# Kernel optimization log

Measured on AMD Instinct MI355X. Metric: run time of the kernel, lower is better.

## Reference

```python
import jax, jax.numpy as jnp
import numpy as np
from jax import lax

NUM_STEPS = 20
BATCH, DIM, HID = 4096, 512, 2048


def setup_inputs() -> dict:
    key = jax.random.key(0)
    k_z, k_w1, k_w2 = jax.random.split(key, 3)
    z0 = jax.random.normal(k_z, (BATCH, DIM), dtype=jnp.float32)
    # fan-in scaled weights so the ODE dynamics stay well-conditioned
    W1 = jax.random.normal(k_w1, (DIM + 1, HID), dtype=jnp.float32) * (1.0 / np.sqrt(DIM + 1))
    b1 = jnp.zeros((HID,), dtype=jnp.float32)
    W2 = jax.random.normal(k_w2, (HID, DIM), dtype=jnp.float32) * (0.1 / np.sqrt(HID))
    b2 = jnp.zeros((DIM,), dtype=jnp.float32)
    t0 = jnp.zeros((), dtype=jnp.float32)
    t1 = jnp.ones((), dtype=jnp.float32)
    return {"z0": z0, "W1": W1, "b1": b1, "W2": W2, "b2": b2, "t0": t0, "t1": t1}


def reference(z0, W1, b1, W2, b2, t0, t1):
    h = (t1 - t0) / NUM_STEPS

    def func(z, t):
        # time broadcast to [batch, 1], concatenated to the state (Neural-ODE MLP dynamics)
        tb = jnp.full((z.shape[0], 1), t, dtype=z.dtype)
        hidden = jnp.tanh(jnp.concatenate([z, tb], axis=-1) @ W1 + b1)
        return hidden @ W2 + b2

    def step(z, i):
        t = t0 + i * h
        k1 = func(z, t)
        k2 = func(z + 0.5 * h * k1, t + 0.5 * h)
        k3 = func(z + 0.5 * h * k2, t + 0.5 * h)
        k4 = func(z + h * k3, t + h)
        z_next = z + (h / 6.0) * (k1 + 2.0 * k2 + 2.0 * k3 + k4)
        return z_next, None

    z, _ = lax.scan(step, z0, jnp.arange(NUM_STEPS, dtype=z0.dtype))
    return z
```

## Files before the change

kernel.cpp:

```cpp
#include <hip/hip_runtime.h>
#include <hip/hip_bf16.h>

#define BATCH 4096
#define DIM   512
#define HID   2048
#define NSTEPS 20

typedef __attribute__((ext_vector_type(8))) short short8;
typedef __attribute__((ext_vector_type(4))) short short4v;
typedef __attribute__((ext_vector_type(4))) float floatx4;

#define GLL(dst, src) __builtin_amdgcn_global_load_lds( \
    (const __attribute__((address_space(1))) void*)(src), \
    (__attribute__((address_space(3))) void*)(dst), 16, 0, 0)

__device__ __forceinline__ short f2bf(float x) {
    union { float f; unsigned u; } v; v.f = x;
    unsigned r = v.u + 0x7fffu + ((v.u >> 16) & 1u);
    return (short)(r >> 16);
}

__device__ __forceinline__ float fast_tanh(float x) {
    float e = __builtin_amdgcn_exp2f(x * 2.8853900817779268f);
    float r = __builtin_amdgcn_rcpf(1.0f + e);
    return 1.0f - 2.0f * r;
}

__global__ void transpose_cvt(const float* __restrict__ src, short* __restrict__ dst,
                              int K, int N) {
    __shared__ float tile[32][33];
    int k0 = blockIdx.x * 32, n0 = blockIdx.y * 32;
    int tx = threadIdx.x, ty = threadIdx.y;
    #pragma unroll
    for (int r = ty; r < 32; r += 8)
        tile[r][tx] = src[(size_t)(k0 + r) * N + n0 + tx];
    __syncthreads();
    #pragma unroll
    for (int r = ty; r < 32; r += 8)
        dst[(size_t)(n0 + r) * K + k0 + tx] = f2bf(tile[tx][r]);
}

__global__ void extract_row(const float* __restrict__ W1, float* __restrict__ w1last) {
    int i = blockIdx.x * 256 + threadIdx.x;
    w1last[i] = W1[(size_t)DIM * HID + i];
}

__global__ void init_abuf(const float* __restrict__ z0, short* __restrict__ abuf) {
    size_t i = (size_t)(blockIdx.x * 256 + threadIdx.x) * 4;
    float4 zv = *(const float4*)(z0 + i);
    short4v o;
    o[0] = f2bf(zv.x); o[1] = f2bf(zv.y); o[2] = f2bf(zv.z); o[3] = f2bf(zv.w);
    *(short4v*)(abuf + i) = o;
}

__global__ __launch_bounds__(256, 4)
void gemm1_tanh(const short* __restrict__ A, const short* __restrict__ Bt,
                const float* __restrict__ b1, const float* __restrict__ w1last,
                const float* __restrict__ t0p, const float* __restrict__ t1p,
                float c_t, float step_i,
                short* __restrict__ hidden) {
    __shared__ short Alds[128 * 64];
    __shared__ short Blds[64 * 64];
    const int tid = threadIdx.x;
    const int lane = tid & 63;
    const int wave = tid >> 6;
    const int wm = wave >> 1, wn = wave & 1;
    const int bm0 = blockIdx.x * 128;
    const int bn0 = blockIdx.y * 64;

    const float t0 = t0p[0], t1 = t1p[0];
    const float h = (t1 - t0) / (float)NSTEPS;
    const float teval = t0 + (step_i + c_t) * h;

    floatx4 acc[4][2];
    #pragma unroll
    for (int i = 0; i < 4; i++) {
        acc[i][0] = (floatx4)0.f;
        acc[i][1] = (floatx4)0.f;
    }

    const int fr = lane & 15;
    const int fkc = lane >> 4;
    const int rx = fr & 7;

    for (int kk = 0; kk < DIM; kk += 64) {
        #pragma unroll
        for (int p = 0; p < 4; p++) {
            int c = tid + p * 256;
            int row = c >> 3;
            int g = (c & 7) ^ (row & 7);
            GLL(&Alds[c * 8], A + (size_t)(bm0 + row) * DIM + kk + g * 8);
        }
        #pragma unroll
        for (int p = 0; p < 2; p++) {
            int c = tid + p * 256;
            int row = c >> 3;
            int g = (c & 7) ^ (row & 7);
            GLL(&Blds[c * 8], Bt + (size_t)(bn0 + row) * DIM + kk + g * 8);
        }
        __syncthreads();
        #pragma unroll
        for (int s = 0; s < 2; s++) {
            const int slot = ((s * 4 + fkc) ^ rx) * 8;
            short8 bfr[2];
            #pragma unroll
            for (int nt = 0; nt < 2; nt++)
                bfr[nt] = *(const short8*)&Blds[(wn * 32 + nt * 16 + fr) * 64 + slot];
            #pragma unroll
            for (int mt = 0; mt < 4; mt++) {
                short8 af = *(const short8*)&Alds[(wm * 64 + mt * 16 + fr) * 64 + slot];
                #pragma unroll
                for (int nt = 0; nt < 2; nt++)
                    acc[mt][nt] = __builtin_amdgcn_mfma_f32_16x16x32_bf16(bfr[nt], af, acc[mt][nt], 0, 0, 0);
            }
        }
        __syncthreads();
    }
    #pragma unroll
    for (int mt = 0; mt < 4; mt++) {
        int m = bm0 + wm * 64 + mt * 16 + fr;
        short* hrow = hidden + (size_t)m * HID;
        #pragma unroll
        for (int nt = 0; nt < 2; nt++) {
            int n0 = bn0 + wn * 32 + nt * 16 + fkc * 4;
            float4 bb = *(const float4*)&b1[n0];
            float4 wl = *(const float4*)&w1last[n0];
            short4v o;
            o[0] = f2bf(fast_tanh(acc[mt][nt][0] + bb.x + teval * wl.x));
            o[1] = f2bf(fast_tanh(acc[mt][nt][1] + bb.y + teval * wl.y));
            o[2] = f2bf(fast_tanh(acc[mt][nt][2] + bb.z + teval * wl.z));
            o[3] = f2bf(fast_tanh(acc[mt][nt][3] + bb.w + teval * wl.w));
            *(short4v*)&hrow[n0] = o;
        }
    }
}

__global__ __launch_bounds__(256, 2)
void gemm2_fused(const short* __restrict__ hidden,
                 const short* __restrict__ Bt,
                 const float* __restrict__ b2,
                 float* __restrict__ z,
                 float* __restrict__ kacc, short* __restrict__ abuf,
                 const float* __restrict__ t0p, const float* __restrict__ t1p,
                 int mode, float wk, float alpha_c) {
    __shared__ short lds[4 * 8192];
    const int tid = threadIdx.x;
    const int lane = tid & 63;
    const int wave = tid >> 6;
    const int bm0 = blockIdx.x * 64;
    const int bn0 = blockIdx.y * 64;
    const int kbase = wave * 512;

    short* slabA = &lds[wave * 8192];
    short* slabB = slabA + 4096;

    const int fr = lane & 15;
    const int fkc = lane >> 4;
    const int rx = fr & 7;
    const int l3 = lane >> 3;
    const int gch = (lane & 7) ^ l3;

    floatx4 acc[4][4];
    #pragma unroll
    for (int i = 0; i < 4; i++)
        #pragma unroll
        for (int j = 0; j < 4; j++) acc[i][j] = (floatx4)0.f;

    for (int kk = 0; kk < 512; kk += 64) {
        const int k0 = kbase + kk;
        __builtin_amdgcn_s_waitcnt(0xC07F);
        #pragma unroll
        for (int j = 0; j < 8; j++) {
            int row = j * 8 + l3;
            GLL(&slabA[j * 512 + lane * 8], hidden + (size_t)(bm0 + row) * HID + k0 + gch * 8);
            GLL(&slabB[j * 512 + lane * 8], Bt     + (size_t)(bn0 + row) * HID + k0 + gch * 8);
        }
        __builtin_amdgcn_sched_barrier(0);
        __builtin_amdgcn_s_waitcnt(0x0F70);
        __builtin_amdgcn_sched_barrier(0);
        #pragma unroll
        for (int s = 0; s < 2; s++) {
            const int slot = ((s * 4 + fkc) ^ rx) * 8;
            short8 af[4], bfr[4];
            #pragma unroll
            for (int mt = 0; mt < 4; mt++)
                af[mt] = *(const short8*)&slabA[(mt * 16 + fr) * 64 + slot];
            #pragma unroll
            for (int nt = 0; nt < 4; nt++)
                bfr[nt] = *(const short8*)&slabB[(nt * 16 + fr) * 64 + slot];
            #pragma unroll
            for (int mt = 0; mt < 4; mt++)
                #pragma unroll
                for (int nt = 0; nt < 4; nt++)
                    acc[mt][nt] = __builtin_amdgcn_mfma_f32_16x16x32_bf16(af[mt], bfr[nt], acc[mt][nt], 0, 0, 0);
        }
        __builtin_amdgcn_sched_barrier(0);
    }

    float* fslab = (float*)slabA;
    #pragma unroll
    for (int mt = 0; mt < 4; mt++)
        #pragma unroll
        for (int nt = 0; nt < 4; nt++)
            #pragma unroll
            for (int r = 0; r < 4; r++) {
                int row = mt * 16 + fkc * 4 + r;
                int col = nt * 16 + fr;
                fslab[row * 64 + col] = acc[mt][nt][r];
            }
    __syncthreads();

    const int rrow = tid >> 2;
    const int cb = (tid & 3) * 16;
    float4 v[4];
    #pragma unroll
    for (int ch = 0; ch < 4; ch++) v[ch] = make_float4(0.f, 0.f, 0.f, 0.f);
    #pragma unroll
    for (int w = 0; w < 4; w++) {
        const float* fs = (const float*)&lds[w * 8192];
        #pragma unroll
        for (int ch = 0; ch < 4; ch++) {
            float4 p = *(const float4*)&fs[rrow * 64 + cb + ch * 4];
            v[ch].x += p.x; v[ch].y += p.y; v[ch].z += p.z; v[ch].w += p.w;
        }
    }

    const float h = (t1p[0] - t0p[0]) / (float)NSTEPS;
    const float ah = alpha_c * h;
    const float h6 = h / 6.0f;
    const size_t base = (size_t)(bm0 + rrow) * DIM + bn0 + cb;
    #pragma unroll
    for (int ch = 0; ch < 4; ch++) {
        float4 bb = *(const float4*)&b2[bn0 + cb + ch * 4];
        float kv[4] = { v[ch].x + bb.x, v[ch].y + bb.y, v[ch].z + bb.z, v[ch].w + bb.w };
        size_t idx = base + ch * 4;
        float4 zv = *(const float4*)&z[idx];
        float zn[4];
        if (mode == 0) {
            *(float4*)&kacc[idx] = make_float4(kv[0], kv[1], kv[2], kv[3]);
            zn[0] = zv.x + ah * kv[0]; zn[1] = zv.y + ah * kv[1];
            zn[2] = zv.z + ah * kv[2]; zn[3] = zv.w + ah * kv[3];
        } else if (mode == 1) {
            float4 ka = *(const float4*)&kacc[idx];
            *(float4*)&kacc[idx] = make_float4(ka.x + wk * kv[0], ka.y + wk * kv[1],
                                               ka.z + wk * kv[2], ka.w + wk * kv[3]);
            zn[0] = zv.x + ah * kv[0]; zn[1] = zv.y + ah * kv[1];
            zn[2] = zv.z + ah * kv[2]; zn[3] = zv.w + ah * kv[3];
        } else {
            float4 ka = *(const float4*)&kacc[idx];
            zn[0] = zv.x + h6 * (ka.x + kv[0]); zn[1] = zv.y + h6 * (ka.y + kv[1]);
            zn[2] = zv.z + h6 * (ka.z + kv[2]); zn[3] = zv.w + h6 * (ka.w + kv[3]);
            *(float4*)&z[idx] = make_float4(zn[0], zn[1], zn[2], zn[3]);
        }
        short4v o;
        o[0] = f2bf(zn[0]); o[1] = f2bf(zn[1]); o[2] = f2bf(zn[2]); o[3] = f2bf(zn[3]);
        *(short4v*)&abuf[idx] = o;
    }
}

extern "C" void kernel_launch(void* const* d_in, const int* in_sizes, int n_in,
                              void* d_out, int out_size, void* d_ws, size_t ws_size,
                              hipStream_t stream) {
    const float* z0  = (const float*)d_in[0];
    const float* W1  = (const float*)d_in[1];
    const float* b1  = (const float*)d_in[2];
    const float* W2  = (const float*)d_in[3];
    const float* b2  = (const float*)d_in[4];
    const float* t0p = (const float*)d_in[5];
    const float* t1p = (const float*)d_in[6];
    float* z = (float*)d_out;

    char* ws = (char*)d_ws;
    short* W1t    = (short*)(ws);
    short* W2t    = (short*)(ws + (2u << 20));
    float* w1last = (float*)(ws + (4u << 20));
    short* abuf   = (short*)(ws + (4u << 20) + (1u << 16));
    short* hidden = (short*)(ws + (8u << 20) + (1u << 16));
    float* kacc   = (float*)(ws + (24u << 20) + (1u << 16));

    hipMemcpyAsync(z, z0, (size_t)BATCH * DIM * sizeof(float),
                   hipMemcpyDeviceToDevice, stream);
    transpose_cvt<<<dim3(DIM / 32, HID / 32), dim3(32, 8), 0, stream>>>(W1, W1t, DIM, HID);
    transpose_cvt<<<dim3(HID / 32, DIM / 32), dim3(32, 8), 0, stream>>>(W2, W2t, HID, DIM);
    extract_row<<<HID / 256, 256, 0, stream>>>(W1, w1last);
    init_abuf<<<BATCH * DIM / 4 / 256, 256, 0, stream>>>(z0, abuf);

    const dim3 g1(BATCH / 128, HID / 64), g2(BATCH / 64, DIM / 64), b(256);
    for (int i = 0; i < NSTEPS; i++) {
        float fi = (float)i;
        gemm1_tanh<<<g1, b, 0, stream>>>(abuf, W1t, b1, w1last, t0p, t1p, 0.0f, fi, hidden);
        gemm2_fused<<<g2, b, 0, stream>>>(hidden, W2t, b2, z, kacc, abuf, t0p, t1p, 0, 1.0f, 0.5f);
        gemm1_tanh<<<g1, b, 0, stream>>>(abuf, W1t, b1, w1last, t0p, t1p, 0.5f, fi, hidden);
        gemm2_fused<<<g2, b, 0, stream>>>(hidden, W2t, b2, z, kacc, abuf, t0p, t1p, 1, 2.0f, 0.5f);
        gemm1_tanh<<<g1, b, 0, stream>>>(abuf, W1t, b1, w1last, t0p, t1p, 0.5f, fi, hidden);
        gemm2_fused<<<g2, b, 0, stream>>>(hidden, W2t, b2, z, kacc, abuf, t0p, t1p, 1, 2.0f, 1.0f);
        gemm1_tanh<<<g1, b, 0, stream>>>(abuf, W1t, b1, w1last, t0p, t1p, 1.0f, fi, hidden);
        gemm2_fused<<<g2, b, 0, stream>>>(hidden, W2t, b2, z, kacc, abuf, t0p, t1p, 2, 1.0f, 0.0f);
    }
}
```

Baseline: 3.145 ms.

## Enlarge gemm1 tiles to 128x128x128 and split gemm2 K across eight waves

gemm1_tanh now computes a 128x128 output tile per block with a 128-wide K step, so each wave holds a 4x4 MFMA accumulator grid. This raises arithmetic intensity and halves the number of blocks, at the cost of more LDS (64KB) and registers, which lowers occupancy. gemm2_fused now uses 512 threads with eight waves each covering 256 of K instead of four covering 512, with an eight-way LDS reduction. That shortens the serial per-wave K loop, adds reduction work, and doubles the LDS footprint.

```diff
diff --git a/kernel.cpp b/kernel.cpp
--- a/kernel.cpp
+++ b/kernel.cpp
@@ -53,66 +53,62 @@
     *(short4v*)(abuf + i) = o;
 }
 
-__global__ __launch_bounds__(256, 4)
+__global__ __launch_bounds__(256, 2)
 void gemm1_tanh(const short* __restrict__ A, const short* __restrict__ Bt,
                 const float* __restrict__ b1, const float* __restrict__ w1last,
                 const float* __restrict__ t0p, const float* __restrict__ t1p,
                 float c_t, float step_i,
                 short* __restrict__ hidden) {
-    __shared__ short Alds[128 * 64];
-    __shared__ short Blds[64 * 64];
+    __shared__ short Alds[128 * 128];
+    __shared__ short Blds[128 * 128];
     const int tid = threadIdx.x;
     const int lane = tid & 63;
     const int wave = tid >> 6;
     const int wm = wave >> 1, wn = wave & 1;
     const int bm0 = blockIdx.x * 128;
-    const int bn0 = blockIdx.y * 64;
+    const int bn0 = blockIdx.y * 128;
 
     const float t0 = t0p[0], t1 = t1p[0];
     const float h = (t1 - t0) / (float)NSTEPS;
     const float teval = t0 + (step_i + c_t) * h;
 
-    floatx4 acc[4][2];
-    #pragma unroll
-    for (int i = 0; i < 4; i++) {
-        acc[i][0] = (floatx4)0.f;
-        acc[i][1] = (floatx4)0.f;
-    }
+    floatx4 acc[4][4];
+    #pragma unroll
+    for (int i = 0; i < 4; i++)
+        #pragma unroll
+        for (int j = 0; j < 4; j++) acc[i][j] = (floatx4)0.f;
 
     const int fr = lane & 15;
     const int fkc = lane >> 4;
     const int rx = fr & 7;
 
-    for (int kk = 0; kk < DIM; kk += 64) {
-        #pragma unroll
-        for (int p = 0; p < 4; p++) {
+    for (int kk = 0; kk < DIM; kk += 128) {
+        #pragma unroll
+        for (int p = 0; p < 8; p++) {
             int c = tid + p * 256;
-            int row = c >> 3;
-            int g = (c & 7) ^ (row & 7);
-            GLL(&Alds[c * 8], A + (size_t)(bm0 + row) * DIM + kk + g * 8);
-        }
-        #pragma unroll
-        for (int p = 0; p < 2; p++) {
-            int c = tid + p * 256;
-            int row = c >> 3;
-            int g = (c & 7) ^ (row & 7);
+            int row = c >> 4;
+            int ci = c & 15;
+            int g = ((ci & 7) ^ (row & 7)) | (ci & 8);
+            GLL(&Alds[c * 8], A  + (size_t)(bm0 + row) * DIM + kk + g * 8);
             GLL(&Blds[c * 8], Bt + (size_t)(bn0 + row) * DIM + kk + g * 8);
         }
         __syncthreads();
         #pragma unroll
-        for (int s = 0; s < 2; s++) {
-            const int slot = ((s * 4 + fkc) ^ rx) * 8;
-            short8 bfr[2];
-            #pragma unroll
-            for (int nt = 0; nt < 2; nt++)
-                bfr[nt] = *(const short8*)&Blds[(wn * 32 + nt * 16 + fr) * 64 + slot];
-            #pragma unroll
-            for (int mt = 0; mt < 4; mt++) {
-                short8 af = *(const short8*)&Alds[(wm * 64 + mt * 16 + fr) * 64 + slot];
+        for (int s = 0; s < 4; s++) {
+            const int lc = s * 4 + fkc;
+            const int slot = ((((lc & 7) ^ rx) | (lc & 8))) * 8;
+            short8 af[4], bfr[4];
+            #pragma unroll
+            for (int mt = 0; mt < 4; mt++)
+                af[mt] = *(const short8*)&Alds[(wm * 64 + mt * 16 + fr) * 128 + slot];
+            #pragma unroll
+            for (int nt = 0; nt < 4; nt++)
+                bfr[nt] = *(const short8*)&Blds[(wn * 64 + nt * 16 + fr) * 128 + slot];
+            #pragma unroll
+            for (int mt = 0; mt < 4; mt++)
                 #pragma unroll
-                for (int nt = 0; nt < 2; nt++)
-                    acc[mt][nt] = __builtin_amdgcn_mfma_f32_16x16x32_bf16(bfr[nt], af, acc[mt][nt], 0, 0, 0);
-            }
+                for (int nt = 0; nt < 4; nt++)
+                    acc[mt][nt] = __builtin_amdgcn_mfma_f32_16x16x32_bf16(bfr[nt], af[mt], acc[mt][nt], 0, 0, 0);
         }
         __syncthreads();
     }
@@ -121,8 +117,8 @@
         int m = bm0 + wm * 64 + mt * 16 + fr;
         short* hrow = hidden + (size_t)m * HID;
         #pragma unroll
-        for (int nt = 0; nt < 2; nt++) {
-            int n0 = bn0 + wn * 32 + nt * 16 + fkc * 4;
+        for (int nt = 0; nt < 4; nt++) {
+            int n0 = bn0 + wn * 64 + nt * 16 + fkc * 4;
             float4 bb = *(const float4*)&b1[n0];
             float4 wl = *(const float4*)&w1last[n0];
             short4v o;
@@ -135,7 +131,7 @@
     }
 }
 
-__global__ __launch_bounds__(256, 2)
+__global__ __launch_bounds__(512, 2)
 void gemm2_fused(const short* __restrict__ hidden,
                  const short* __restrict__ Bt,
                  const float* __restrict__ b2,
@@ -143,13 +139,13 @@
                  float* __restrict__ kacc, short* __restrict__ abuf,
                  const float* __restrict__ t0p, const float* __restrict__ t1p,
                  int mode, float wk, float alpha_c) {
-    __shared__ short lds[4 * 8192];
+    __shared__ short lds[8 * 8192];
     const int tid = threadIdx.x;
     const int lane = tid & 63;
     const int wave = tid >> 6;
     const int bm0 = blockIdx.x * 64;
     const int bn0 = blockIdx.y * 64;
-    const int kbase = wave * 512;
+    const int kbase = wave * 256;
 
     short* slabA = &lds[wave * 8192];
     short* slabB = slabA + 4096;
@@ -166,8 +162,9 @@
         #pragma unroll
         for (int j = 0; j < 4; j++) acc[i][j] = (floatx4)0.f;
 
-    for (int kk = 0; kk < 512; kk += 64) {
-        const int k0 = kbase + kk;
+    #pragma unroll
+    for (int it = 0; it < 4; ++it) {
+        const int k0 = kbase + it * 64;
         __builtin_amdgcn_s_waitcnt(0xC07F);
         #pragma unroll
         for (int j = 0; j < 8; j++) {
@@ -210,52 +207,59 @@
             }
     __syncthreads();
 
-    const int rrow = tid >> 2;
-    const int cb = (tid & 3) * 16;
-    float4 v[4];
-    #pragma unroll
-    for (int ch = 0; ch < 4; ch++) v[ch] = make_float4(0.f, 0.f, 0.f, 0.f);
-    #pragma unroll
-    for (int w = 0; w < 4; w++) {
+    const int rrow = tid >> 3;
+    const int c8 = (tid & 7) * 8;
+    float4 v0 = make_float4(0.f, 0.f, 0.f, 0.f);
+    float4 v1 = make_float4(0.f, 0.f, 0.f, 0.f);
+    #pragma unroll
+    for (int w = 0; w < 8; w++) {
         const float* fs = (const float*)&lds[w * 8192];
-        #pragma unroll
-        for (int ch = 0; ch < 4; ch++) {
-            float4 p = *(const float4*)&fs[rrow * 64 + cb + ch * 4];
-            v[ch].x += p.x; v[ch].y += p.y; v[ch].z += p.z; v[ch].w += p.w;
-        }
+        float4 p0 = *(const float4*)&fs[rrow * 64 + c8];
+        float4 p1 = *(const float4*)&fs[rrow * 64 + c8 + 4];
+        v0.x += p0.x; v0.y += p0.y; v0.z += p0.z; v0.w += p0.w;
+        v1.x += p1.x; v1.y += p1.y; v1.z += p1.z; v1.w += p1.w;
     }
 
     const float h = (t1p[0] - t0p[0]) / (float)NSTEPS;
     const float ah = alpha_c * h;
     const float h6 = h / 6.0f;
-    const size_t base = (size_t)(bm0 + rrow) * DIM + bn0 + cb;
-    #pragma unroll
-    for (int ch = 0; ch < 4; ch++) {
-        float4 bb = *(const float4*)&b2[bn0 + cb + ch * 4];
-        float kv[4] = { v[ch].x + bb.x, v[ch].y + bb.y, v[ch].z + bb.z, v[ch].w + bb.w };
-        size_t idx = base + ch * 4;
-        float4 zv = *(const float4*)&z[idx];
-        float zn[4];
-        if (mode == 0) {
-            *(float4*)&kacc[idx] = make_float4(kv[0], kv[1], kv[2], kv[3]);
-            zn[0] = zv.x + ah * kv[0]; zn[1] = zv.y + ah * kv[1];
-            zn[2] = zv.z + ah * kv[2]; zn[3] = zv.w + ah * kv[3];
-        } else if (mode == 1) {
-            float4 ka = *(const float4*)&kacc[idx];
-            *(float4*)&kacc[idx] = make_float4(ka.x + wk * kv[0], ka.y + wk * kv[1],
-                                               ka.z + wk * kv[2], ka.w + wk * kv[3]);
-            zn[0] = zv.x + ah * kv[0]; zn[1] = zv.y + ah * kv[1];
-            zn[2] = zv.z + ah * kv[2]; zn[3] = zv.w + ah * kv[3];
-        } else {
-            float4 ka = *(const float4*)&kacc[idx];
-            zn[0] = zv.x + h6 * (ka.x + kv[0]); zn[1] = zv.y + h6 * (ka.y + kv[1]);
-            zn[2] = zv.z + h6 * (ka.z + kv[2]); zn[3] = zv.w + h6 * (ka.w + kv[3]);
-            *(float4*)&z[idx] = make_float4(zn[0], zn[1], zn[2], zn[3]);
-        }
-        short4v o;
-        o[0] = f2bf(zn[0]); o[1] = f2bf(zn[1]); o[2] = f2bf(zn[2]); o[3] = f2bf(zn[3]);
-        *(short4v*)&abuf[idx] = o;
-    }
+    const size_t base = (size_t)(bm0 + rrow) * DIM + bn0 + c8;
+    float4 bb0 = *(const float4*)&b2[bn0 + c8];
+    float4 bb1 = *(const float4*)&b2[bn0 + c8 + 4];
+    float kv[8] = { v0.x + bb0.x, v0.y + bb0.y, v0.z + bb0.z, v0.w + bb0.w,
+                    v1.x + bb1.x, v1.y + bb1.y, v1.z + bb1.z, v1.w + bb1.w };
+    float4 zv0 = *(const float4*)&z[base];
+    float4 zv1 = *(const float4*)&z[base + 4];
+    float zl[8] = { zv0.x, zv0.y, zv0.z, zv0.w, zv1.x, zv1.y, zv1.z, zv1.w };
+    float zn[8];
+    if (mode == 0) {
+        *(float4*)&kacc[base]     = make_float4(kv[0], kv[1], kv[2], kv[3]);
+        *(float4*)&kacc[base + 4] = make_float4(kv[4], kv[5], kv[6], kv[7]);
+        #pragma unroll
+        for (int i = 0; i < 8; i++) zn[i] = zl[i] + ah * kv[i];
+    } else if (mode == 1) {
+        float4 ka0 = *(const float4*)&kacc[base];
+        float4 ka1 = *(const float4*)&kacc[base + 4];
+        *(float4*)&kacc[base]     = make_float4(ka0.x + wk * kv[0], ka0.y + wk * kv[1],
+                                                ka0.z + wk * kv[2], ka0.w + wk * kv[3]);
+        *(float4*)&kacc[base + 4] = make_float4(ka1.x + wk * kv[4], ka1.y + wk * kv[5],
+                                                ka1.z + wk * kv[6], ka1.w + wk * kv[7]);
+        #pragma unroll
+        for (int i = 0; i < 8; i++) zn[i] = zl[i] + ah * kv[i];
+    } else {
+        float4 ka0 = *(const float4*)&kacc[base];
+        float4 ka1 = *(const float4*)&kacc[base + 4];
+        float kaf[8] = { ka0.x, ka0.y, ka0.z, ka0.w, ka1.x, ka1.y, ka1.z, ka1.w };
+        #pragma unroll
+        for (int i = 0; i < 8; i++) zn[i] = zl[i] + h6 * (kaf[i] + kv[i]);
+        *(float4*)&z[base]     = make_float4(zn[0], zn[1], zn[2], zn[3]);
+        *(float4*)&z[base + 4] = make_float4(zn[4], zn[5], zn[6], zn[7]);
+    }
+    short4v o0, o1;
+    o0[0] = f2bf(zn[0]); o0[1] = f2bf(zn[1]); o0[2] = f2bf(zn[2]); o0[3] = f2bf(zn[3]);
+    o1[0] = f2bf(zn[4]); o1[1] = f2bf(zn[5]); o1[2] = f2bf(zn[6]); o1[3] = f2bf(zn[7]);
+    *(short4v*)&abuf[base]     = o0;
+    *(short4v*)&abuf[base + 4] = o1;
 }
 
 extern "C" void kernel_launch(void* const* d_in, const int* in_sizes, int n_in,
@@ -285,16 +289,17 @@
     extract_row<<<HID / 256, 256, 0, stream>>>(W1, w1last);
     init_abuf<<<BATCH * DIM / 4 / 256, 256, 0, stream>>>(z0, abuf);
 
-    const dim3 g1(BATCH / 128, HID / 64), g2(BATCH / 64, DIM / 64), b(256);
+    const dim3 g1(BATCH / 128, HID / 128), g2(BATCH / 64, DIM / 64);
+    const dim3 b1d(256), b2d(512);
     for (int i = 0; i < NSTEPS; i++) {
         float fi = (float)i;
-        gemm1_tanh<<<g1, b, 0, stream>>>(abuf, W1t, b1, w1last, t0p, t1p, 0.0f, fi, hidden);
-        gemm2_fused<<<g2, b, 0, stream>>>(hidden, W2t, b2, z, kacc, abuf, t0p, t1p, 0, 1.0f, 0.5f);
-        gemm1_tanh<<<g1, b, 0, stream>>>(abuf, W1t, b1, w1last, t0p, t1p, 0.5f, fi, hidden);
-        gemm2_fused<<<g2, b, 0, stream>>>(hidden, W2t, b2, z, kacc, abuf, t0p, t1p, 1, 2.0f, 0.5f);
-        gemm1_tanh<<<g1, b, 0, stream>>>(abuf, W1t, b1, w1last, t0p, t1p, 0.5f, fi, hidden);
-        gemm2_fused<<<g2, b, 0, stream>>>(hidden, W2t, b2, z, kacc, abuf, t0p, t1p, 1, 2.0f, 1.0f);
-        gemm1_tanh<<<g1, b, 0, stream>>>(abuf, W1t, b1, w1last, t0p, t1p, 1.0f, fi, hidden);
-        gemm2_fused<<<g2, b, 0, stream>>>(hidden, W2t, b2, z, kacc, abuf, t0p, t1p, 2, 1.0f, 0.0f);
-    }
-}
+        gemm1_tanh<<<g1, b1d, 0, stream>>>(abuf, W1t, b1, w1last, t0p, t1p, 0.0f, fi, hidden);
+        gemm2_fused<<<g2, b2d, 0, stream>>>(hidden, W2t, b2, z, kacc, abuf, t0p, t1p, 0, 1.0f, 0.5f);
+        gemm1_tanh<<<g1, b1d, 0, stream>>>(abuf, W1t, b1, w1last, t0p, t1p, 0.5f, fi, hidden);
+        gemm2_fused<<<g2, b2d, 0, stream>>>(hidden, W2t, b2, z, kacc, abuf, t0p, t1p, 1, 2.0f, 0.5f);
+        gemm1_tanh<<<g1, b1d, 0, stream>>>(abuf, W1t, b1, w1last, t0p, t1p, 0.5f, fi, hidden);
+        gemm2_fused<<<g2, b2d, 0, stream>>>(hidden, W2t, b2, z, kacc, abuf, t0p, t1p, 1, 2.0f, 1.0f);
+        gemm1_tanh<<<g1, b1d, 0, stream>>>(abuf, W1t, b1, w1last, t0p, t1p, 1.0f, fi, hidden);
+        gemm2_fused<<<g2, b2d, 0, stream>>>(hidden, W2t, b2, z, kacc, abuf, t0p, t1p, 2, 1.0f, 0.0f);
+    }
+}
```

Result: faster. 3.021 ms, median of 2 (-3.9%).
